# Optimization experiments

Hardware: AMD Instinct MI355X
Metric: run time of the kernel (lower is better)

Reference implementation:

```python
import jax, jax.numpy as jnp
import numpy as np

NEG_SLOPE = 0.2  # PyG GATv2Conv default negative_slope
N_NODES = 50000
N_EDGES = 600000
N_GRAPHS = 512


def gatv2_layer(x, src, dst, Wl, bl, Wr, br, att, bias, n_nodes, heads, out_ch):
    """PyG GATv2Conv (concat=False -> mean over heads). src/dst include self-loops."""
    xl = (x @ Wl + bl).reshape(n_nodes, heads, out_ch)  # source transform
    xr = (x @ Wr + br).reshape(n_nodes, heads, out_ch)  # target transform
    e = jax.nn.leaky_relu(xl[src] + xr[dst], NEG_SLOPE)          # [E, H, C]
    logits = jnp.einsum('ehc,hc->eh', e, att)                     # [E, H]
    # segment softmax over destination node
    amax = jax.ops.segment_max(logits, dst, num_segments=n_nodes)  # [N, H]
    amax = jnp.where(jnp.isfinite(amax), amax, 0.0)
    ex = jnp.exp(logits - amax[dst])
    denom = jax.ops.segment_sum(ex, dst, num_segments=n_nodes)
    alpha = ex / jnp.clip(denom[dst], 1e-16)                      # [E, H]
    msg = xl[src] * alpha[:, :, None]                             # [E, H, C]
    out = jax.ops.segment_sum(msg, dst, num_segments=n_nodes)     # [N, H, C]
    return out.mean(axis=1) + bias                                # [N, C]


def setup_inputs() -> dict:
    key = jax.random.key(0)
    ks = jax.random.split(key, 20)
    s = 0.1
    x = jax.random.normal(ks[0], (N_NODES, 7), dtype=jnp.float32)
    edge_index = jax.random.randint(ks[1], (2, N_EDGES), 0, N_NODES, dtype=jnp.int64)
    batch = jnp.sort(jax.random.randint(ks[2], (N_NODES,), 0, N_GRAPHS, dtype=jnp.int64))
    H1, C1 = 2, 64   # conv1: 7 -> 64, heads=2
    H2, C2 = 2, 64   # conv2: 64 -> 64, heads=2
    H3, C3 = 1, 128  # conv3: 64 -> 128, heads=1
    p = {
        'W1l': jax.random.normal(ks[3], (7, H1 * C1)) * s,
        'b1l': jnp.zeros((H1 * C1,), jnp.float32),
        'W1r': jax.random.normal(ks[4], (7, H1 * C1)) * s,
        'b1r': jnp.zeros((H1 * C1,), jnp.float32),
        'att1': jax.random.normal(ks[5], (H1, C1)) * s,
        'bias1': jnp.zeros((C1,), jnp.float32),
        'W2l': jax.random.normal(ks[6], (C1, H2 * C2)) * s,
        'b2l': jnp.zeros((H2 * C2,), jnp.float32),
        'W2r': jax.random.normal(ks[7], (C1, H2 * C2)) * s,
        'b2r': jnp.zeros((H2 * C2,), jnp.float32),
        'att2': jax.random.normal(ks[8], (H2, C2)) * s,
        'bias2': jnp.zeros((C2,), jnp.float32),
        'W3l': jax.random.normal(ks[9], (C2, H3 * C3)) * s,
        'b3l': jnp.zeros((H3 * C3,), jnp.float32),
        'W3r': jax.random.normal(ks[10], (C2, H3 * C3)) * s,
        'b3r': jnp.zeros((H3 * C3,), jnp.float32),
        'att3': jax.random.normal(ks[11], (H3, C3)) * s,
        'bias3': jnp.zeros((C3,), jnp.float32),
        'Wc': jax.random.normal(ks[12], (C3, 11)) * s,
        'bc': jnp.zeros((11,), jnp.float32),
    }
    return {'x': x, 'edge_index': edge_index, 'batch': batch, **p}


def reference(x, edge_index, batch,
              W1l, b1l, W1r, b1r, att1, bias1,
              W2l, b2l, W2r, b2r, att2, bias2,
              W3l, b3l, W3r, b3r, att3, bias3,
              Wc, bc):
    n = x.shape[0]
    # GATv2Conv default add_self_loops=True (same augmented edge set each layer)
    loop = jnp.arange(n, dtype=edge_index.dtype)
    src = jnp.concatenate([edge_index[0], loop])
    dst = jnp.concatenate([edge_index[1], loop])

    h = jax.nn.elu(gatv2_layer(x, src, dst, W1l, b1l, W1r, b1r, att1, bias1, n, 2, 64))
    h = jax.nn.elu(gatv2_layer(h, src, dst, W2l, b2l, W2r, b2r, att2, bias2, n, 2, 64))
    h = gatv2_layer(h, src, dst, W3l, b3l, W3r, b3r, att3, bias3, n, 1, 128)

    # global mean pool over graphs
    sums = jax.ops.segment_sum(h, batch, num_segments=N_GRAPHS)          # [G, 128]
    cnt = jax.ops.segment_sum(jnp.ones((n,), h.dtype), batch, num_segments=N_GRAPHS)
    graph_embed = sums / jnp.clip(cnt, 1.0)[:, None]
    return graph_embed @ Wc + bc                                         # [G, 11]
```

## Files before the change

### kernel.cpp

```cpp
#include <hip/hip_runtime.h>
#include <hip/hip_bf16.h>
#include <math.h>


#define PAD_SHIFT 6


__global__ void build_csr(const int* __restrict__ edge_src, const int* __restrict__ edge_dst,
                          int* __restrict__ cnt, int* __restrict__ csr, int NE, int E) {
    int e = blockIdx.x * blockDim.x + threadIdx.x;
    if (e >= E) return;
    int s, d;
    if (e < NE) { s = edge_src[e]; d = edge_dst[e]; }
    else        { s = d = e - NE; }
    int pos = atomicAdd(&cnt[d], 1) & 63;
    csr[(d << PAD_SHIFT) + pos] = s;
}


template<int IN_CH, int NPW>
__global__ __launch_bounds__(256) void transform_tile(
        const float* __restrict__ in,
        const float* __restrict__ Wl, const float* __restrict__ bl,
        const float* __restrict__ Wr, const float* __restrict__ br,
        float* __restrict__ xl, float* __restrict__ xr, int n) {
    constexpr int NPB = 4 * NPW;
    __shared__ alignas(16) float rows[NPB][IN_CH];
    int tid = threadIdx.x;
    int t = tid & 63, w = tid >> 6;
    int n0 = blockIdx.x * NPB;

    if constexpr (IN_CH % 4 == 0) {
        constexpr int K4 = IN_CH / 4;
        for (int idx = tid; idx < NPB * K4; idx += 256) {
            int nn = idx / K4, k4 = idx - nn * K4;
            int node = n0 + nn; if (node > n - 1) node = n - 1;
            ((float4*)rows[nn])[k4] = ((const float4*)(in + (size_t)node * IN_CH))[k4];
        }
    } else {
        for (int idx = tid; idx < NPB * IN_CH; idx += 256) {
            int nn = idx / IN_CH, k = idx - nn * IN_CH;
            int node = n0 + nn; if (node > n - 1) node = n - 1;
            rows[nn][k] = in[(size_t)node * IN_CH + k];
        }
    }
    __syncthreads();

    int nb = w * NPW;
    float accl0[NPW], accl1[NPW], accr0[NPW], accr1[NPW];
    float bl0 = bl[t], bl1 = bl[t + 64], br0 = br[t], br1 = br[t + 64];
#pragma unroll
    for (int nn = 0; nn < NPW; ++nn) {
        accl0[nn] = bl0; accl1[nn] = bl1; accr0[nn] = br0; accr1[nn] = br1;
    }

    if constexpr (IN_CH % 4 == 0) {
        constexpr int K4 = IN_CH / 4;
        for (int k4 = 0; k4 < K4; ++k4) {
            float wl0[4], wl1[4], wr0[4], wr1[4];
#pragma unroll
            for (int j = 0; j < 4; ++j) {
                wl0[j] = Wl[(k4 * 4 + j) * 128 + t];
                wl1[j] = Wl[(k4 * 4 + j) * 128 + t + 64];
                wr0[j] = Wr[(k4 * 4 + j) * 128 + t];
                wr1[j] = Wr[(k4 * 4 + j) * 128 + t + 64];
            }
#pragma unroll
            for (int nn = 0; nn < NPW; ++nn) {
                float4 r = ((const float4*)rows[nb + nn])[k4];
                accl0[nn] = fmaf(r.x, wl0[0], accl0[nn]);
                accl1[nn] = fmaf(r.x, wl1[0], accl1[nn]);
                accr0[nn] = fmaf(r.x, wr0[0], accr0[nn]);
                accr1[nn] = fmaf(r.x, wr1[0], accr1[nn]);
                accl0[nn] = fmaf(r.y, wl0[1], accl0[nn]);
                accl1[nn] = fmaf(r.y, wl1[1], accl1[nn]);
                accr0[nn] = fmaf(r.y, wr0[1], accr0[nn]);
                accr1[nn] = fmaf(r.y, wr1[1], accr1[nn]);
                accl0[nn] = fmaf(r.z, wl0[2], accl0[nn]);
                accl1[nn] = fmaf(r.z, wl1[2], accl1[nn]);
                accr0[nn] = fmaf(r.z, wr0[2], accr0[nn]);
                accr1[nn] = fmaf(r.z, wr1[2], accr1[nn]);
                accl0[nn] = fmaf(r.w, wl0[3], accl0[nn]);
                accl1[nn] = fmaf(r.w, wl1[3], accl1[nn]);
                accr0[nn] = fmaf(r.w, wr0[3], accr0[nn]);
                accr1[nn] = fmaf(r.w, wr1[3], accr1[nn]);
            }
        }
    } else {
#pragma unroll
        for (int k = 0; k < IN_CH; ++k) {
            float wl0 = Wl[k * 128 + t], wl1 = Wl[k * 128 + t + 64];
            float wr0 = Wr[k * 128 + t], wr1 = Wr[k * 128 + t + 64];
#pragma unroll
            for (int nn = 0; nn < NPW; ++nn) {
                float xv = rows[nb + nn][k];
                accl0[nn] = fmaf(xv, wl0, accl0[nn]);
                accl1[nn] = fmaf(xv, wl1, accl1[nn]);
                accr0[nn] = fmaf(xv, wr0, accr0[nn]);
                accr1[nn] = fmaf(xv, wr1, accr1[nn]);
            }
        }
    }

#pragma unroll
    for (int nn = 0; nn < NPW; ++nn) {
        int node = n0 + nb + nn;
        if (node < n) {
            float* ol  = xl + ((size_t)node << 7);
            float* orr = xr + ((size_t)node << 7);
            ol[t] = accl0[nn]; ol[t + 64] = accl1[nn];
            orr[t] = accr0[nn]; orr[t + 64] = accr1[nn];
        }
    }
}


template<int CTRL>
__device__ __forceinline__ float dpp_add(float v) {
    int x = __builtin_amdgcn_update_dpp(0, __float_as_int(v), CTRL, 0xF, 0xF, true);
    return v + __int_as_float(x);
}
__device__ __forceinline__ float reduce16(float v) {
    v = dpp_add<0xB1>(v);
    v = dpp_add<0x4E>(v);
    v = dpp_add<0x141>(v);
    v = dpp_add<0x140>(v);
    return v;
}


__device__ __forceinline__ float chan4(float p, const float4& c, const float4& xv,
                                       const float4& a, const float4& a2) {
    float t;
    t = c.x + xv.x; p = fmaf(t > 0.f ? a.x : a2.x, t, p);
    t = c.y + xv.y; p = fmaf(t > 0.f ? a.y : a2.y, t, p);
    t = c.z + xv.z; p = fmaf(t > 0.f ? a.z : a2.z, t, p);
    t = c.w + xv.w; p = fmaf(t > 0.f ? a.w : a2.w, t, p);
    return p;
}
__device__ __forceinline__ void acc4(float4& a, float w, const float4& c) {
    a.x = fmaf(w, c.x, a.x); a.y = fmaf(w, c.y, a.y);
    a.z = fmaf(w, c.z, a.z); a.w = fmaf(w, c.w, a.w);
}


#define AGG_PH(C0, C1, F0, F1)                                                 \
    {                                                                          \
        int tf0 = srcof(it + 2 * EPI + eg);                                    \
        int tf1 = srcof(it + 2 * EPI + STEP + eg);                             \
        const float4* f0p = (const float4*)(xl + ((size_t)tf0 << 7) + rowo);   \
        const float4* f1p = (const float4*)(xl + ((size_t)tf1 << 7) + rowo);   \
        F0[0] = f0p[0]; F0[1] = f1p[0];                                        \
        if constexpr (!TWOHEAD) { F1[0] = f0p[16]; F1[1] = f1p[16]; }          \
        bool v0 = (it + eg) < deg, v1 = (it + STEP + eg) < deg;                \
        float pa = chan4(0.f, C0[0], xrv0, atv0, atw0);                        \
        float pb = chan4(0.f, C0[1], xrv0, atv0, atw0);                        \
        if constexpr (!TWOHEAD) {                                              \
            pa = chan4(pa, C1[0], xrv1, atv1, atw1);                           \
            pb = chan4(pb, C1[1], xrv1, atv1, atw1);                           \
        }                                                                      \
        pa = reduce16(pa); pb = reduce16(pb);                                  \
        float w0 = v0 ? exp2f(pa) : 0.f;                                       \
        float w1 = v1 ? exp2f(pb) : 0.f;                                       \
        ssum += w0 + w1;                                                       \
        acc4(acc0, w0, C0[0]); acc4(acc0, w1, C0[1]);                          \
        if constexpr (!TWOHEAD) { acc4(acc1, w0, C1[0]); acc4(acc1, w1, C1[1]); } \
        it += EPI;                                                             \
    }

template<bool TWOHEAD>
__global__ void gat_agg_fused(const float* __restrict__ xl, const float* __restrict__ xr,
                              const float* __restrict__ att, const float* __restrict__ bias,
                              const int* __restrict__ cnt, const int* __restrict__ csr,
                              float* __restrict__ outbuf, int n) {
    constexpr int STEP = TWOHEAD ? 2 : 4;
    constexpr int EPI  = 2 * STEP;
    constexpr float L2E = 1.4426950408889634f;
    int wid = (blockIdx.x * blockDim.x + threadIdx.x) >> 6;
    if (wid >= n) return;
    int node = wid;
    int lane = threadIdx.x & 63;
    int g = lane >> 4, q = lane & 15;
    int eg   = TWOHEAD ? (g >> 1) : g;
    int head = TWOHEAD ? (g & 1)  : 0;
    int rowo = TWOHEAD ? (head * 64 + q * 4) : (q * 4);

    const float4* xr4 = (const float4*)(xr + ((size_t)node << 7) + rowo);
    float4 xrv0 = xr4[0], xrv1;
    const float4* at4 = (const float4*)(att + rowo);
    float4 atv0 = at4[0], atv1, atw0, atw1;
    atv0.x *= L2E; atv0.y *= L2E; atv0.z *= L2E; atv0.w *= L2E;
    atw0.x = 0.2f * atv0.x; atw0.y = 0.2f * atv0.y;
    atw0.z = 0.2f * atv0.z; atw0.w = 0.2f * atv0.w;
    if constexpr (!TWOHEAD) {
        xrv1 = xr4[16]; atv1 = at4[16];
        atv1.x *= L2E; atv1.y *= L2E; atv1.z *= L2E; atv1.w *= L2E;
        atw1.x = 0.2f * atv1.x; atw1.y = 0.2f * atv1.y;
        atw1.z = 0.2f * atv1.z; atw1.w = 0.2f * atv1.w;
    }

    int deg = cnt[node]; if (deg > 64) deg = 64;
    int idxvec = csr[((size_t)node << PAD_SHIFT) + lane];
    auto srcof = [&](int p) { return __shfl(idxvec, p < deg ? p : 0, 64); };

    float4 X0[2], X1[2], Y0[2], Y1[2], Z0[2], Z1[2];
    {
        int s00 = srcof(eg), s01 = srcof(STEP + eg);
        int s10 = srcof(EPI + eg), s11 = srcof(EPI + STEP + eg);
        const float4* p00 = (const float4*)(xl + ((size_t)s00 << 7) + rowo);
        const float4* p01 = (const float4*)(xl + ((size_t)s01 << 7) + rowo);
        const float4* p10 = (const float4*)(xl + ((size_t)s10 << 7) + rowo);
        const float4* p11 = (const float4*)(xl + ((size_t)s11 << 7) + rowo);
        X0[0] = p00[0]; X0[1] = p01[0];
        Y0[0] = p10[0]; Y0[1] = p11[0];
        if constexpr (!TWOHEAD) {
            X1[0] = p00[16]; X1[1] = p01[16];
            Y1[0] = p10[16]; Y1[1] = p11[16];
        }
    }

    float ssum = 0.f;
    float4 acc0 = {0,0,0,0}, acc1 = {0,0,0,0};
    int it = 0;
    while (true) {
        AGG_PH(X0, X1, Z0, Z1)
        if (it >= deg) break;
        AGG_PH(Y0, Y1, X0, X1)
        if (it >= deg) break;
        AGG_PH(Z0, Z1, Y0, Y1)
        if (it >= deg) break;
    }

    {
        ssum  += __shfl_xor(ssum, 32, 64);
        acc0.x += __shfl_xor(acc0.x, 32, 64); acc0.y += __shfl_xor(acc0.y, 32, 64);
        acc0.z += __shfl_xor(acc0.z, 32, 64); acc0.w += __shfl_xor(acc0.w, 32, 64);
        if constexpr (!TWOHEAD) {
            acc1.x += __shfl_xor(acc1.x, 32, 64); acc1.y += __shfl_xor(acc1.y, 32, 64);
            acc1.z += __shfl_xor(acc1.z, 32, 64); acc1.w += __shfl_xor(acc1.w, 32, 64);
            ssum  += __shfl_xor(ssum, 16, 64);
            acc0.x += __shfl_xor(acc0.x, 16, 64); acc0.y += __shfl_xor(acc0.y, 16, 64);
            acc0.z += __shfl_xor(acc0.z, 16, 64); acc0.w += __shfl_xor(acc0.w, 16, 64);
            acc1.x += __shfl_xor(acc1.x, 16, 64); acc1.y += __shfl_xor(acc1.y, 16, 64);
            acc1.z += __shfl_xor(acc1.z, 16, 64); acc1.w += __shfl_xor(acc1.w, 16, 64);
        }
    }

    float inv = 1.f / ssum;
    if constexpr (TWOHEAD) {
        float4 r;
        r.x = acc0.x * inv; r.y = acc0.y * inv; r.z = acc0.z * inv; r.w = acc0.w * inv;
        float4 ro;
        ro.x = __shfl_xor(r.x, 16, 64); ro.y = __shfl_xor(r.y, 16, 64);
        ro.z = __shfl_xor(r.z, 16, 64); ro.w = __shfl_xor(r.w, 16, 64);
        float4 bv = ((const float4*)bias)[q];
        float4 o;
        o.x = 0.5f * (r.x + ro.x) + bv.x;
        o.y = 0.5f * (r.y + ro.y) + bv.y;
        o.z = 0.5f * (r.z + ro.z) + bv.z;
        o.w = 0.5f * (r.w + ro.w) + bv.w;
        o.x = (o.x > 0.f) ? o.x : expm1f(o.x);
        o.y = (o.y > 0.f) ? o.y : expm1f(o.y);
        o.z = (o.z > 0.f) ? o.z : expm1f(o.z);
        o.w = (o.w > 0.f) ? o.w : expm1f(o.w);
        if (lane < 16) ((float4*)(outbuf + (size_t)node * 64))[q] = o;
    } else {
        float4 bv0 = ((const float4*)bias)[q];
        float4 bv1 = ((const float4*)bias)[q + 16];
        float4 r0, r1;
        r0.x = acc0.x * inv + bv0.x; r0.y = acc0.y * inv + bv0.y;
        r0.z = acc0.z * inv + bv0.z; r0.w = acc0.w * inv + bv0.w;
        r1.x = acc1.x * inv + bv1.x; r1.y = acc1.y * inv + bv1.y;
        r1.z = acc1.z * inv + bv1.z; r1.w = acc1.w * inv + bv1.w;
        if (lane < 16) {
            ((float4*)(outbuf + ((size_t)node << 7)))[q]      = r0;
            ((float4*)(outbuf + ((size_t)node << 7)))[q + 16] = r1;
        }
    }
}


__device__ __forceinline__ int lower_bound(const int* __restrict__ a, int n, int key) {
    int lo = 0, hi = n;
    while (lo < hi) {
        int mid = (lo + hi) >> 1;
        if (a[mid] < key) lo = mid + 1; else hi = mid;
    }
    return lo;
}

__global__ void pool_kernel(const float* __restrict__ h3, const int* __restrict__ batch,
                            const float* __restrict__ Wc, const float* __restrict__ bc,
                            float* __restrict__ out, int n, int G) {
    int g = blockIdx.x;
    int tid = threadIdx.x;
    __shared__ float mean[128];
    int start = lower_bound(batch, n, g);
    int end   = lower_bound(batch, n, g + 1);
    float s0 = 0.f, s1 = 0.f, s2 = 0.f, s3 = 0.f;
    int node = start;
    for (; node + 3 < end; node += 4) {
        s0 += h3[(size_t)node * 128 + tid];
        s1 += h3[(size_t)(node + 1) * 128 + tid];
        s2 += h3[(size_t)(node + 2) * 128 + tid];
        s3 += h3[(size_t)(node + 3) * 128 + tid];
    }
    for (; node < end; ++node) s0 += h3[(size_t)node * 128 + tid];
    float s = (s0 + s1) + (s2 + s3);
    int cnt = end - start;
    float mv = s / (float)(cnt > 0 ? cnt : 1);
    mean[tid] = mv;
    __syncthreads();
    if (tid < 11) {
        float o = bc[tid];
        for (int c = 0; c < 128; ++c) o += mean[c] * Wc[c * 11 + tid];
        out[g * 11 + tid] = o;
    }
}


extern "C" void kernel_launch(void* const* d_in, const int* in_sizes, int n_in,
                              void* d_out, int out_size, void* d_ws, size_t ws_size,
                              hipStream_t stream) {
    const float* x     = (const float*)d_in[0];
    const int*   ei    = (const int*)d_in[1];
    const int*   batch = (const int*)d_in[2];
    const float* W1l = (const float*)d_in[3],  *b1l = (const float*)d_in[4];
    const float* W1r = (const float*)d_in[5],  *b1r = (const float*)d_in[6];
    const float* att1 = (const float*)d_in[7], *bias1 = (const float*)d_in[8];
    const float* W2l = (const float*)d_in[9],  *b2l = (const float*)d_in[10];
    const float* W2r = (const float*)d_in[11], *b2r = (const float*)d_in[12];
    const float* att2 = (const float*)d_in[13], *bias2 = (const float*)d_in[14];
    const float* W3l = (const float*)d_in[15], *b3l = (const float*)d_in[16];
    const float* W3r = (const float*)d_in[17], *b3r = (const float*)d_in[18];
    const float* att3 = (const float*)d_in[19], *bias3 = (const float*)d_in[20];
    const float* Wc  = (const float*)d_in[21], *bc  = (const float*)d_in[22];
    float* out = (float*)d_out;

    const int N  = in_sizes[0] / 7;
    const int NE = in_sizes[1] / 2;
    const int E  = NE + N;
    const int G  = out_size / 11;

    const int* edge_src = ei;
    const int* edge_dst = ei + NE;

    char* p = (char*)d_ws;
    auto alloc = [&](size_t bytes) { void* r = (void*)p; p += (bytes + 255) & ~(size_t)255; return r; };
    int*   cnt     = (int*)alloc((size_t)N * sizeof(int));
    int*   csr     = (int*)alloc((size_t)N * 64 * sizeof(int));
    float* xl      = (float*)alloc((size_t)N * 128 * sizeof(float));
    float* xr      = (float*)alloc((size_t)N * 128 * sizeof(float));
    float* hbuf    = (float*)alloc((size_t)N * 128 * sizeof(float));

    (void)hipMemsetAsync(cnt, 0, (size_t)N * sizeof(int), stream);
    build_csr<<<(E + 255) / 256, 256, 0, stream>>>(edge_src, edge_dst, cnt, csr, NE, E);

    const int NPB = 32;
    int tgrid = (N + NPB - 1) / NPB;
    int agrid = (N + 3) / 4;

    transform_tile<7, 8><<<tgrid, 256, 0, stream>>>(x, W1l, b1l, W1r, b1r, xl, xr, N);
    gat_agg_fused<true><<<agrid, 256, 0, stream>>>(xl, xr, att1, bias1, cnt, csr, hbuf, N);

    transform_tile<64, 8><<<tgrid, 256, 0, stream>>>(hbuf, W2l, b2l, W2r, b2r, xl, xr, N);
    gat_agg_fused<true><<<agrid, 256, 0, stream>>>(xl, xr, att2, bias2, cnt, csr, hbuf, N);

    transform_tile<64, 8><<<tgrid, 256, 0, stream>>>(hbuf, W3l, b3l, W3r, b3r, xl, xr, N);
    gat_agg_fused<false><<<agrid, 256, 0, stream>>>(xl, xr, att3, bias3, cnt, csr, hbuf, N);

    pool_kernel<<<G, 128, 0, stream>>>(hbuf, batch, Wc, bc, out, N, G);
}
```

Baseline: 282.8 us.

## Store source-transformed features as bf16 and regather with 8-channel lanes

The transform kernel now writes xl (the per-source features gathered once per edge) as bf16 instead of fp32, which halves the bytes moved by the random edge gathers in each aggregation. The aggregation kernel is restructured so each lane holds 8 contiguous channels loaded with a single 16-byte load and unpacked from bf16. Four edges are processed per wave step for all head counts, with reduction widths adjusted per head. This trades reduced precision in xl (used in both attention logits and messages) for lower gather bandwidth.

```diff
diff --git a/kernel.cpp b/kernel.cpp
--- a/kernel.cpp
+++ b/kernel.cpp
@@ -23,7 +23,7 @@
         const float* __restrict__ in,
         const float* __restrict__ Wl, const float* __restrict__ bl,
         const float* __restrict__ Wr, const float* __restrict__ br,
-        float* __restrict__ xl, float* __restrict__ xr, int n) {
+        ushort* __restrict__ xlh, float* __restrict__ xr, int n) {
     constexpr int NPB = 4 * NPW;
     __shared__ alignas(16) float rows[NPB][IN_CH];
     int tid = threadIdx.x;
@@ -106,9 +106,10 @@
     for (int nn = 0; nn < NPW; ++nn) {
         int node = n0 + nb + nn;
         if (node < n) {
-            float* ol  = xl + ((size_t)node << 7);
+            __hip_bfloat16* hl = (__hip_bfloat16*)(xlh + ((size_t)node << 7));
             float* orr = xr + ((size_t)node << 7);
-            ol[t] = accl0[nn]; ol[t + 64] = accl1[nn];
+            hl[t]      = __float2bfloat16(accl0[nn]);
+            hl[t + 64] = __float2bfloat16(accl1[nn]);
             orr[t] = accr0[nn]; orr[t + 64] = accr1[nn];
         }
     }
@@ -120,161 +121,137 @@
     int x = __builtin_amdgcn_update_dpp(0, __float_as_int(v), CTRL, 0xF, 0xF, true);
     return v + __int_as_float(x);
 }
-__device__ __forceinline__ float reduce16(float v) {
+__device__ __forceinline__ float reduce8(float v) {
     v = dpp_add<0xB1>(v);
     v = dpp_add<0x4E>(v);
     v = dpp_add<0x141>(v);
+    return v;
+}
+__device__ __forceinline__ float reduce16(float v) {
+    v = reduce8(v);
     v = dpp_add<0x140>(v);
     return v;
 }
 
 
-__device__ __forceinline__ float chan4(float p, const float4& c, const float4& xv,
-                                       const float4& a, const float4& a2) {
-    float t;
-    t = c.x + xv.x; p = fmaf(t > 0.f ? a.x : a2.x, t, p);
-    t = c.y + xv.y; p = fmaf(t > 0.f ? a.y : a2.y, t, p);
-    t = c.z + xv.z; p = fmaf(t > 0.f ? a.z : a2.z, t, p);
-    t = c.w + xv.w; p = fmaf(t > 0.f ? a.w : a2.w, t, p);
-    return p;
-}
-__device__ __forceinline__ void acc4(float4& a, float w, const float4& c) {
-    a.x = fmaf(w, c.x, a.x); a.y = fmaf(w, c.y, a.y);
-    a.z = fmaf(w, c.z, a.z); a.w = fmaf(w, c.w, a.w);
-}
-
-
-#define AGG_PH(C0, C1, F0, F1)                                                 \
+__device__ __forceinline__ void unpack8(const uint4& u, float c[8]) {
+    c[0] = __int_as_float((int)(u.x << 16));
+    c[1] = __int_as_float((int)(u.x & 0xffff0000u));
+    c[2] = __int_as_float((int)(u.y << 16));
+    c[3] = __int_as_float((int)(u.y & 0xffff0000u));
+    c[4] = __int_as_float((int)(u.z << 16));
+    c[5] = __int_as_float((int)(u.z & 0xffff0000u));
+    c[6] = __int_as_float((int)(u.w << 16));
+    c[7] = __int_as_float((int)(u.w & 0xffff0000u));
+}
+
+
+#define AGG_PH(CUR, FRE)                                                       \
     {                                                                          \
-        int tf0 = srcof(it + 2 * EPI + eg);                                    \
-        int tf1 = srcof(it + 2 * EPI + STEP + eg);                             \
-        const float4* f0p = (const float4*)(xl + ((size_t)tf0 << 7) + rowo);   \
-        const float4* f1p = (const float4*)(xl + ((size_t)tf1 << 7) + rowo);   \
-        F0[0] = f0p[0]; F0[1] = f1p[0];                                        \
-        if constexpr (!TWOHEAD) { F1[0] = f0p[16]; F1[1] = f1p[16]; }          \
-        bool v0 = (it + eg) < deg, v1 = (it + STEP + eg) < deg;                \
-        float pa = chan4(0.f, C0[0], xrv0, atv0, atw0);                        \
-        float pb = chan4(0.f, C0[1], xrv0, atv0, atw0);                        \
-        if constexpr (!TWOHEAD) {                                              \
-            pa = chan4(pa, C1[0], xrv1, atv1, atw1);                           \
-            pb = chan4(pb, C1[1], xrv1, atv1, atw1);                           \
+        int tf0 = srcof(it + 2 * EPI + g);                                     \
+        int tf1 = srcof(it + 2 * EPI + 4 + g);                                 \
+        FRE[0] = *(const uint4*)(xlh + ((size_t)tf0 << 7) + (q << 3));         \
+        FRE[1] = *(const uint4*)(xlh + ((size_t)tf1 << 7) + (q << 3));         \
+        _Pragma("unroll")                                                      \
+        for (int j = 0; j < 2; ++j) {                                          \
+            float c[8]; unpack8(CUR[j], c);                                    \
+            float p = 0.f;                                                     \
+            _Pragma("unroll")                                                  \
+            for (int k = 0; k < 8; ++k) {                                      \
+                float tt = c[k] + xrv[k];                                      \
+                p = fmaf(tt > 0.f ? atv[k] : atw[k], tt, p);                   \
+            }                                                                  \
+            p = TWOHEAD ? reduce8(p) : reduce16(p);                            \
+            float w = (it + j * 4 + g) < deg ? exp2f(p) : 0.f;                 \
+            ssum += w;                                                         \
+            _Pragma("unroll")                                                  \
+            for (int k = 0; k < 8; ++k) acc[k] = fmaf(w, c[k], acc[k]);        \
         }                                                                      \
-        pa = reduce16(pa); pb = reduce16(pb);                                  \
-        float w0 = v0 ? exp2f(pa) : 0.f;                                       \
-        float w1 = v1 ? exp2f(pb) : 0.f;                                       \
-        ssum += w0 + w1;                                                       \
-        acc4(acc0, w0, C0[0]); acc4(acc0, w1, C0[1]);                          \
-        if constexpr (!TWOHEAD) { acc4(acc1, w0, C1[0]); acc4(acc1, w1, C1[1]); } \
         it += EPI;                                                             \
     }
 
 template<bool TWOHEAD>
-__global__ void gat_agg_fused(const float* __restrict__ xl, const float* __restrict__ xr,
+__global__ void gat_agg_fused(const ushort* __restrict__ xlh, const float* __restrict__ xr,
                               const float* __restrict__ att, const float* __restrict__ bias,
                               const int* __restrict__ cnt, const int* __restrict__ csr,
                               float* __restrict__ outbuf, int n) {
-    constexpr int STEP = TWOHEAD ? 2 : 4;
-    constexpr int EPI  = 2 * STEP;
+    constexpr int EPI = 8;
     constexpr float L2E = 1.4426950408889634f;
     int wid = (blockIdx.x * blockDim.x + threadIdx.x) >> 6;
     if (wid >= n) return;
     int node = wid;
     int lane = threadIdx.x & 63;
     int g = lane >> 4, q = lane & 15;
-    int eg   = TWOHEAD ? (g >> 1) : g;
-    int head = TWOHEAD ? (g & 1)  : 0;
-    int rowo = TWOHEAD ? (head * 64 + q * 4) : (q * 4);
-
-    const float4* xr4 = (const float4*)(xr + ((size_t)node << 7) + rowo);
-    float4 xrv0 = xr4[0], xrv1;
-    const float4* at4 = (const float4*)(att + rowo);
-    float4 atv0 = at4[0], atv1, atw0, atw1;
-    atv0.x *= L2E; atv0.y *= L2E; atv0.z *= L2E; atv0.w *= L2E;
-    atw0.x = 0.2f * atv0.x; atw0.y = 0.2f * atv0.y;
-    atw0.z = 0.2f * atv0.z; atw0.w = 0.2f * atv0.w;
-    if constexpr (!TWOHEAD) {
-        xrv1 = xr4[16]; atv1 = at4[16];
-        atv1.x *= L2E; atv1.y *= L2E; atv1.z *= L2E; atv1.w *= L2E;
-        atw1.x = 0.2f * atv1.x; atw1.y = 0.2f * atv1.y;
-        atw1.z = 0.2f * atv1.z; atw1.w = 0.2f * atv1.w;
+
+    float xrv[8], atv[8], atw[8], acc[8];
+    {
+        const float4* xp = (const float4*)(xr + ((size_t)node << 7) + q * 8);
+        const float4* ap = (const float4*)(att + q * 8);
+        float4 x0 = xp[0], x1 = xp[1], a0 = ap[0], a1 = ap[1];
+        xrv[0]=x0.x; xrv[1]=x0.y; xrv[2]=x0.z; xrv[3]=x0.w;
+        xrv[4]=x1.x; xrv[5]=x1.y; xrv[6]=x1.z; xrv[7]=x1.w;
+        atv[0]=a0.x*L2E; atv[1]=a0.y*L2E; atv[2]=a0.z*L2E; atv[3]=a0.w*L2E;
+        atv[4]=a1.x*L2E; atv[5]=a1.y*L2E; atv[6]=a1.z*L2E; atv[7]=a1.w*L2E;
+#pragma unroll
+        for (int k = 0; k < 8; ++k) { atw[k] = 0.2f * atv[k]; acc[k] = 0.f; }
     }
 
     int deg = cnt[node]; if (deg > 64) deg = 64;
     int idxvec = csr[((size_t)node << PAD_SHIFT) + lane];
     auto srcof = [&](int p) { return __shfl(idxvec, p < deg ? p : 0, 64); };
 
-    float4 X0[2], X1[2], Y0[2], Y1[2], Z0[2], Z1[2];
+    uint4 X[2], Y[2], Z[2];
     {
-        int s00 = srcof(eg), s01 = srcof(STEP + eg);
-        int s10 = srcof(EPI + eg), s11 = srcof(EPI + STEP + eg);
-        const float4* p00 = (const float4*)(xl + ((size_t)s00 << 7) + rowo);
-        const float4* p01 = (const float4*)(xl + ((size_t)s01 << 7) + rowo);
-        const float4* p10 = (const float4*)(xl + ((size_t)s10 << 7) + rowo);
-        const float4* p11 = (const float4*)(xl + ((size_t)s11 << 7) + rowo);
-        X0[0] = p00[0]; X0[1] = p01[0];
-        Y0[0] = p10[0]; Y0[1] = p11[0];
-        if constexpr (!TWOHEAD) {
-            X1[0] = p00[16]; X1[1] = p01[16];
-            Y1[0] = p10[16]; Y1[1] = p11[16];
-        }
+        int s00 = srcof(g), s01 = srcof(4 + g);
+        int s10 = srcof(EPI + g), s11 = srcof(EPI + 4 + g);
+        X[0] = *(const uint4*)(xlh + ((size_t)s00 << 7) + (q << 3));
+        X[1] = *(const uint4*)(xlh + ((size_t)s01 << 7) + (q << 3));
+        Y[0] = *(const uint4*)(xlh + ((size_t)s10 << 7) + (q << 3));
+        Y[1] = *(const uint4*)(xlh + ((size_t)s11 << 7) + (q << 3));
     }
 
     float ssum = 0.f;
-    float4 acc0 = {0,0,0,0}, acc1 = {0,0,0,0};
     int it = 0;
     while (true) {
-        AGG_PH(X0, X1, Z0, Z1)
+        AGG_PH(X, Z)
         if (it >= deg) break;
-        AGG_PH(Y0, Y1, X0, X1)
+        AGG_PH(Y, X)
         if (it >= deg) break;
-        AGG_PH(Z0, Z1, Y0, Y1)
+        AGG_PH(Z, Y)
         if (it >= deg) break;
     }
 
-    {
-        ssum  += __shfl_xor(ssum, 32, 64);
-        acc0.x += __shfl_xor(acc0.x, 32, 64); acc0.y += __shfl_xor(acc0.y, 32, 64);
-        acc0.z += __shfl_xor(acc0.z, 32, 64); acc0.w += __shfl_xor(acc0.w, 32, 64);
-        if constexpr (!TWOHEAD) {
-            acc1.x += __shfl_xor(acc1.x, 32, 64); acc1.y += __shfl_xor(acc1.y, 32, 64);
-            acc1.z += __shfl_xor(acc1.z, 32, 64); acc1.w += __shfl_xor(acc1.w, 32, 64);
-            ssum  += __shfl_xor(ssum, 16, 64);
-            acc0.x += __shfl_xor(acc0.x, 16, 64); acc0.y += __shfl_xor(acc0.y, 16, 64);
-            acc0.z += __shfl_xor(acc0.z, 16, 64); acc0.w += __shfl_xor(acc0.w, 16, 64);
-            acc1.x += __shfl_xor(acc1.x, 16, 64); acc1.y += __shfl_xor(acc1.y, 16, 64);
-            acc1.z += __shfl_xor(acc1.z, 16, 64); acc1.w += __shfl_xor(acc1.w, 16, 64);
-        }
+    ssum += __shfl_xor(ssum, 32, 64);
+    ssum += __shfl_xor(ssum, 16, 64);
+#pragma unroll
+    for (int k = 0; k < 8; ++k) {
+        acc[k] += __shfl_xor(acc[k], 32, 64);
+        acc[k] += __shfl_xor(acc[k], 16, 64);
     }
 
     float inv = 1.f / ssum;
     if constexpr (TWOHEAD) {
-        float4 r;
-        r.x = acc0.x * inv; r.y = acc0.y * inv; r.z = acc0.z * inv; r.w = acc0.w * inv;
-        float4 ro;
-        ro.x = __shfl_xor(r.x, 16, 64); ro.y = __shfl_xor(r.y, 16, 64);
-        ro.z = __shfl_xor(r.z, 16, 64); ro.w = __shfl_xor(r.w, 16, 64);
-        float4 bv = ((const float4*)bias)[q];
-        float4 o;
-        o.x = 0.5f * (r.x + ro.x) + bv.x;
-        o.y = 0.5f * (r.y + ro.y) + bv.y;
-        o.z = 0.5f * (r.z + ro.z) + bv.z;
-        o.w = 0.5f * (r.w + ro.w) + bv.w;
-        o.x = (o.x > 0.f) ? o.x : expm1f(o.x);
-        o.y = (o.y > 0.f) ? o.y : expm1f(o.y);
-        o.z = (o.z > 0.f) ? o.z : expm1f(o.z);
-        o.w = (o.w > 0.f) ? o.w : expm1f(o.w);
-        if (lane < 16) ((float4*)(outbuf + (size_t)node * 64))[q] = o;
+        float o[8];
+#pragma unroll
+        for (int k = 0; k < 8; ++k) {
+            float r = acc[k] * inv;
+            float ro = __shfl_xor(r, 8, 64);
+            float v = 0.5f * (r + ro) + bias[(q & 7) * 8 + k];
+            o[k] = (v > 0.f) ? v : expm1f(v);
+        }
+        if (lane < 8) {
+            float4* op = (float4*)(outbuf + (size_t)node * 64 + q * 8);
+            op[0] = make_float4(o[0], o[1], o[2], o[3]);
+            op[1] = make_float4(o[4], o[5], o[6], o[7]);
+        }
     } else {
-        float4 bv0 = ((const float4*)bias)[q];
-        float4 bv1 = ((const float4*)bias)[q + 16];
-        float4 r0, r1;
-        r0.x = acc0.x * inv + bv0.x; r0.y = acc0.y * inv + bv0.y;
-        r0.z = acc0.z * inv + bv0.z; r0.w = acc0.w * inv + bv0.w;
-        r1.x = acc1.x * inv + bv1.x; r1.y = acc1.y * inv + bv1.y;
-        r1.z = acc1.z * inv + bv1.z; r1.w = acc1.w * inv + bv1.w;
+        float o[8];
+#pragma unroll
+        for (int k = 0; k < 8; ++k) o[k] = acc[k] * inv + bias[q * 8 + k];
         if (lane < 16) {
-            ((float4*)(outbuf + ((size_t)node << 7)))[q]      = r0;
-            ((float4*)(outbuf + ((size_t)node << 7)))[q + 16] = r1;
+            float4* op = (float4*)(outbuf + ((size_t)node << 7) + q * 8);
+            op[0] = make_float4(o[0], o[1], o[2], o[3]);
+            op[1] = make_float4(o[4], o[5], o[6], o[7]);
         }
     }
 }
@@ -347,11 +324,11 @@
 
     char* p = (char*)d_ws;
     auto alloc = [&](size_t bytes) { void* r = (void*)p; p += (bytes + 255) & ~(size_t)255; return r; };
-    int*   cnt     = (int*)alloc((size_t)N * sizeof(int));
-    int*   csr     = (int*)alloc((size_t)N * 64 * sizeof(int));
-    float* xl      = (float*)alloc((size_t)N * 128 * sizeof(float));
-    float* xr      = (float*)alloc((size_t)N * 128 * sizeof(float));
-    float* hbuf    = (float*)alloc((size_t)N * 128 * sizeof(float));
+    int*    cnt  = (int*)alloc((size_t)N * sizeof(int));
+    int*    csr  = (int*)alloc((size_t)N * 64 * sizeof(int));
+    ushort* xlh  = (ushort*)alloc((size_t)N * 128 * sizeof(ushort));
+    float*  xr   = (float*)alloc((size_t)N * 128 * sizeof(float));
+    float*  hbuf = (float*)alloc((size_t)N * 128 * sizeof(float));
 
     (void)hipMemsetAsync(cnt, 0, (size_t)N * sizeof(int), stream);
     build_csr<<<(E + 255) / 256, 256, 0, stream>>>(edge_src, edge_dst, cnt, csr, NE, E);
@@ -360,14 +337,14 @@
     int tgrid = (N + NPB - 1) / NPB;
     int agrid = (N + 3) / 4;
 
-    transform_tile<7, 8><<<tgrid, 256, 0, stream>>>(x, W1l, b1l, W1r, b1r, xl, xr, N);
-    gat_agg_fused<true><<<agrid, 256, 0, stream>>>(xl, xr, att1, bias1, cnt, csr, hbuf, N);
-
-    transform_tile<64, 8><<<tgrid, 256, 0, stream>>>(hbuf, W2l, b2l, W2r, b2r, xl, xr, N);
-    gat_agg_fused<true><<<agrid, 256, 0, stream>>>(xl, xr, att2, bias2, cnt, csr, hbuf, N);
-
-    transform_tile<64, 8><<<tgrid, 256, 0, stream>>>(hbuf, W3l, b3l, W3r, b3r, xl, xr, N);
-    gat_agg_fused<false><<<agrid, 256, 0, stream>>>(xl, xr, att3, bias3, cnt, csr, hbuf, N);
+    transform_tile<7, 8><<<tgrid, 256, 0, stream>>>(x, W1l, b1l, W1r, b1r, xlh, xr, N);
+    gat_agg_fused<true><<<agrid, 256, 0, stream>>>(xlh, xr, att1, bias1, cnt, csr, hbuf, N);
+
+    transform_tile<64, 8><<<tgrid, 256, 0, stream>>>(hbuf, W2l, b2l, W2r, b2r, xlh, xr, N);
+    gat_agg_fused<true><<<agrid, 256, 0, stream>>>(xlh, xr, att2, bias2, cnt, csr, hbuf, N);
+
+    transform_tile<64, 8><<<tgrid, 256, 0, stream>>>(hbuf, W3l, b3l, W3r, b3r, xlh, xr, N);
+    gat_agg_fused<false><<<agrid, 256, 0, stream>>>(xlh, xr, att3, bias3, cnt, csr, hbuf, N);
 
     pool_kernel<<<G, 128, 0, stream>>>(hbuf, batch, Wc, bc, out, N, G);
 }
```

Result: no change. 283.5 us (+0.3%).
